# Optimization experiments

Measured on AMD Instinct MI355X. Metric: run time of the kernel, lower is better.

## Reference

```python
import jax, jax.numpy as jnp
import numpy as np

D_MODEL = 1024
N_HEADS = 16
D_HEAD = D_MODEL // N_HEADS
B, T = 4, 2048


def setup_inputs() -> dict:
    key = jax.random.key(0)
    k1, k2, k3 = jax.random.split(key, 3)
    x = jax.random.normal(k1, (B, T, D_MODEL), dtype=jnp.float32)
    # match nn.Linear init scale roughly (uniform ~ 1/sqrt(fan_in)); scale normal for stability
    w_qkv = jax.random.normal(k2, (D_MODEL, 3 * D_MODEL), dtype=jnp.float32) / np.sqrt(D_MODEL)
    w_out = jax.random.normal(k3, (D_MODEL, D_MODEL), dtype=jnp.float32) / np.sqrt(D_MODEL)
    return {"x": x, "w_qkv": w_qkv, "w_out": w_out}


def reference(x, w_qkv, w_out):
    Bx, Tx, D = x.shape
    H, Dh = N_HEADS, D_HEAD
    qkv = x @ w_qkv                                  # [B,T,3D]
    qkv = qkv.reshape(Bx, Tx, 3, H, Dh)
    q, k, v = qkv[:, :, 0], qkv[:, :, 1], qkv[:, :, 2]  # [B,T,H,Dh]
    scores = jnp.einsum('bqhd,bkhd->bhqk', q, k) / np.sqrt(Dh).astype(np.float32)
    mask = jnp.triu(jnp.ones((Tx, Tx), dtype=bool), k=1)  # causal: mask future
    scores = jnp.where(mask, -jnp.inf, scores)
    attn = jax.nn.softmax(scores, axis=-1)
    out = jnp.einsum('bhqk,bkhd->bqhd', attn, v).reshape(Bx, Tx, D)
    return out @ w_out
```

## Files before the change

### kernel.cpp

```cpp
#include <hip/hip_runtime.h>
#include <math.h>

#define T_SEQ 2048
#define NB 4
#define NH 16
#define DH 64
#define DM 1024

typedef __attribute__((ext_vector_type(8))) __bf16 bf16x8;
typedef __attribute__((ext_vector_type(4))) float f32x4;

typedef const __attribute__((address_space(1))) void* gas_t;
typedef __attribute__((address_space(3))) void* las_t;

#if __has_builtin(__builtin_amdgcn_exp2f)
#define EXP2(x) __builtin_amdgcn_exp2f(x)
#else
#define EXP2(x) __expf((x) * 0.69314718056f)
#endif

__device__ inline bool detect_f32(const unsigned short* probe, int lane) {
    unsigned short u = probe[lane];
    int e = (u >> 7) & 0xFF;
    bool outlier = (e >= 140) || (e <= 90 && (u & 0x7fff) != 0);
    unsigned long long m = __ballot(outlier);
    return __popcll(m) >= 4;
}

__device__ inline bf16x8 load8_flex(const void* base, long elem, bool f32) {
    if (!f32) {
        return *(const bf16x8*)((const __bf16*)base + elem);
    } else {
        const float* f = (const float*)base + elem;
        float4 a = *(const float4*)f;
        float4 b = *(const float4*)(f + 4);
        bf16x8 r;
        r[0] = (__bf16)a.x; r[1] = (__bf16)a.y; r[2] = (__bf16)a.z; r[3] = (__bf16)a.w;
        r[4] = (__bf16)b.x; r[5] = (__bf16)b.y; r[6] = (__bf16)b.z; r[7] = (__bf16)b.w;
        return r;
    }
}

__global__ __launch_bounds__(256)
void cvt_x(const float* __restrict__ in, __bf16* __restrict__ out, long n8) {
    long i = (long)blockIdx.x * blockDim.x + threadIdx.x;
    if (i >= n8) return;
    const float* f = in + i * 8;
    float4 a = *(const float4*)f;
    float4 b = *(const float4*)(f + 4);
    bf16x8 r;
    r[0] = (__bf16)a.x; r[1] = (__bf16)a.y; r[2] = (__bf16)a.z; r[3] = (__bf16)a.w;
    r[4] = (__bf16)b.x; r[5] = (__bf16)b.y; r[6] = (__bf16)b.z; r[7] = (__bf16)b.w;
    *(bf16x8*)(out + i * 8) = r;
}

__global__ __launch_bounds__(256)
void tpose_cvt(const float* __restrict__ in, __bf16* __restrict__ out, int R, int C) {
    __shared__ __bf16 tile[32][33];
    const int bx = blockIdx.x * 32;
    const int by = blockIdx.y * 32;
    const int tx = threadIdx.x & 31;
    const int ty = threadIdx.x >> 5;
#pragma unroll
    for (int it = 0; it < 4; ++it) {
        int r = ty + it * 8;
        tile[r][tx] = (__bf16)in[(long)(by + r) * C + bx + tx];
    }
    __syncthreads();
#pragma unroll
    for (int it = 0; it < 4; ++it) {
        int r = ty + it * 8;
        out[(long)(bx + r) * R + by + tx] = tile[tx][r];
    }
}

__global__ __launch_bounds__(256)
void gemm_bt(const __bf16* __restrict__ A, long lda,
             const __bf16* __restrict__ Bt, long ldb,
             void* __restrict__ C, long ldc, int c_f32, int K) {
    __shared__ __align__(16) __bf16 sA[128 * 32];
    __shared__ __align__(16) __bf16 sB[128 * 32];
    const int tid  = threadIdx.x;
    const int lane = tid & 63;
    const int wave = tid >> 6;
    const int l15  = lane & 15;
    const int quad = lane >> 4;

    const int wg   = blockIdx.x;
    const int xcd  = wg & 7;
    const int idx  = wg >> 3;
    const int bm = (xcd * 8 + (idx & 7)) * 128;
    const int bn = (idx >> 3) * 128;

    const int wm = (wave & 1) * 64;
    const int wn = (wave >> 1) * 64;

    f32x4 zero = {0.f, 0.f, 0.f, 0.f};
    f32x4 acc[4][4];
#pragma unroll
    for (int i = 0; i < 4; ++i)
#pragma unroll
        for (int j = 0; j < 4; ++j) acc[i][j] = zero;

    const int srow = tid >> 2;
    const int scol = (tid & 3) * 8;
    const __bf16* gA0 = A  + (long)(bm + srow) * lda + scol;
    const __bf16* gA1 = A  + (long)(bm + 64 + srow) * lda + scol;
    const __bf16* gB0 = Bt + (long)(bn + srow) * ldb + scol;
    const __bf16* gB1 = Bt + (long)(bn + 64 + srow) * ldb + scol;

    __bf16* lA0 = sA + wave * 512;
    __bf16* lA1 = sA + 2048 + wave * 512;
    __bf16* lB0 = sB + wave * 512;
    __bf16* lB1 = sB + 2048 + wave * 512;

    for (int k0 = 0; k0 < K; k0 += 32) {
        __syncthreads();
        __builtin_amdgcn_global_load_lds((gas_t)(gA0 + k0), (las_t)lA0, 16, 0, 0);
        __builtin_amdgcn_global_load_lds((gas_t)(gA1 + k0), (las_t)lA1, 16, 0, 0);
        __builtin_amdgcn_global_load_lds((gas_t)(gB0 + k0), (las_t)lB0, 16, 0, 0);
        __builtin_amdgcn_global_load_lds((gas_t)(gB1 + k0), (las_t)lB1, 16, 0, 0);
        __syncthreads();

        bf16x8 af[4], bfm[4];
#pragma unroll
        for (int i = 0; i < 4; ++i)
            af[i] = *(const bf16x8*)(sA + (wm + i * 16 + l15) * 32 + quad * 8);
#pragma unroll
        for (int j = 0; j < 4; ++j)
            bfm[j] = *(const bf16x8*)(sB + (wn + j * 16 + l15) * 32 + quad * 8);
#pragma unroll
        for (int i = 0; i < 4; ++i)
#pragma unroll
            for (int j = 0; j < 4; ++j)
                acc[i][j] = __builtin_amdgcn_mfma_f32_16x16x32_bf16(af[i], bfm[j], acc[i][j], 0, 0, 0);
    }

#pragma unroll
    for (int i = 0; i < 4; ++i)
#pragma unroll
        for (int j = 0; j < 4; ++j)
#pragma unroll
            for (int r = 0; r < 4; ++r) {
                int row = bm + wm + i * 16 + quad * 4 + r;
                int col = bn + wn + j * 16 + l15;
                if (c_f32)
                    ((float*)C)[(long)row * ldc + col] = acc[i][j][r];
                else
                    ((__bf16*)C)[(long)row * ldc + col] = (__bf16)acc[i][j][r];
            }
}

__global__ __launch_bounds__(256)
void gemm_bn(const void* __restrict__ A, long lda, long a0, int a_flex,
             const void* __restrict__ B, long ldb, int b_flex,
             void* __restrict__ C, long ldc, int c_flex, int K,
             const unsigned short* __restrict__ probe) {
    __shared__ __align__(16) __bf16 sA[128 * 32];
    __shared__ __align__(16) __bf16 sB[128 * 32];
    const int tid  = threadIdx.x;
    const int lane = tid & 63;
    const int wave = tid >> 6;
    const int l15  = lane & 15;
    const int quad = lane >> 4;
    const int bm = blockIdx.y * 128;
    const int bn = blockIdx.x * 128;
    const int wm = (wave & 1) * 64;
    const int wn = (wave >> 1) * 64;

    const bool is_f32 = detect_f32(probe, lane);
    const bool a_f32 = a_flex && is_f32;
    const bool b_f32 = b_flex && is_f32;
    const bool c_f32 = c_flex && is_f32;

    f32x4 zero = {0.f, 0.f, 0.f, 0.f};
    f32x4 acc[4][4];
#pragma unroll
    for (int i = 0; i < 4; ++i)
#pragma unroll
        for (int j = 0; j < 4; ++j) acc[i][j] = zero;

    const int srow = tid >> 2;
    const int scol = (tid & 3) * 8;

    for (int k0 = 0; k0 < K; k0 += 32) {
        __syncthreads();
        *(bf16x8*)(sA + tid * 8) =
            load8_flex(A, a0 + (long)(bm + srow) * lda + k0 + scol, a_f32);
        *(bf16x8*)(sA + 2048 + tid * 8) =
            load8_flex(A, a0 + (long)(bm + 64 + srow) * lda + k0 + scol, a_f32);
#pragma unroll
        for (int it = 0; it < 2; ++it) {
            int idx = tid + it * 256;
            int kk  = idx & 31;
            int n8  = (idx >> 5) * 8;
            bf16x8 bv = load8_flex(B, (long)(k0 + kk) * ldb + bn + n8, b_f32);
#pragma unroll
            for (int jj = 0; jj < 8; ++jj) sB[(n8 + jj) * 32 + kk] = bv[jj];
        }
        __syncthreads();

        bf16x8 af[4], bfm[4];
#pragma unroll
        for (int i = 0; i < 4; ++i)
            af[i] = *(const bf16x8*)(sA + (wm + i * 16 + l15) * 32 + quad * 8);
#pragma unroll
        for (int j = 0; j < 4; ++j)
            bfm[j] = *(const bf16x8*)(sB + (wn + j * 16 + l15) * 32 + quad * 8);
#pragma unroll
        for (int i = 0; i < 4; ++i)
#pragma unroll
            for (int j = 0; j < 4; ++j)
                acc[i][j] = __builtin_amdgcn_mfma_f32_16x16x32_bf16(af[i], bfm[j], acc[i][j], 0, 0, 0);
    }

#pragma unroll
    for (int i = 0; i < 4; ++i)
#pragma unroll
        for (int j = 0; j < 4; ++j)
#pragma unroll
            for (int r = 0; r < 4; ++r) {
                int row = bm + wm + i * 16 + quad * 4 + r;
                int col = bn + wn + j * 16 + l15;
                if (c_f32)
                    ((float*)C)[(long)row * ldc + col] = acc[i][j][r];
                else
                    ((__bf16*)C)[(long)row * ldc + col] = (__bf16)acc[i][j][r];
            }
}

__global__ __launch_bounds__(512, 4)
void attn_k(__bf16* __restrict__ qkvp, int bhbits) {
    const int bid  = blockIdx.x;
    const int p    = bid >> bhbits;
    const int bh   = bid & ((1 << bhbits) - 1);
    const int h    = bh & 15;
    const int b    = bh >> 4;
    const int tid  = threadIdx.x;
    const int lane = tid & 63;
    const int wave = tid >> 6;
    const int l15  = lane & 15;
    const int quad = lane >> 4;

    __shared__ __align__(16) __bf16 sK[64 * 72];
    __shared__ __align__(16) __bf16 sVT[64 * 64];
    __shared__ __align__(16) __bf16 sP[8][16 * 64];

    const long rs = 3 * DM;
    __bf16* base = qkvp + (long)b * T_SEQ * rs + h * DH;

    const int sr  = tid >> 3;
    const int sm  = tid & 7;
    const int sc8 = sm * 8;
    const int rot = 8 * ((5 * sm) & 7);
    const int vcol = (sr + rot) & 63;

    bf16x8 vone;
#pragma unroll
    for (int jj = 0; jj < 8; ++jj) vone[jj] = (__bf16)1.0f;

    f32x4 zero = {0.f, 0.f, 0.f, 0.f};

#pragma unroll 1
    for (int half = 0; half < 2; ++half) {
        const int qt  = half ? (15 - p) : p;
        const int q0  = qt * 128;
        const int wq0 = q0 + wave * 16;
        const int nk  = (q0 + 128) >> 6;

        const float qscale = 0.125f * 1.44269504089f;
        bf16x8 qa[2];
#pragma unroll
        for (int kk = 0; kk < 2; ++kk) {
            bf16x8 v = *(const bf16x8*)(base + (long)(wq0 + l15) * rs + kk * 32 + quad * 8);
#pragma unroll
            for (int jj = 0; jj < 8; ++jj) v[jj] = (__bf16)((float)v[jj] * qscale);
            qa[kk] = v;
        }

        f32x4 o[4], o4;
        o4 = zero;
#pragma unroll
        for (int j = 0; j < 4; ++j) o[j] = zero;

        bf16x8 kreg, vreg;
        {
            const __bf16* rp = base + (long)sr * rs;
            kreg = *(const bf16x8*)(rp + DM + sc8);
            vreg = *(const bf16x8*)(rp + 2 * DM + sc8);
        }

        for (int t = 0; t < nk; ++t) {
            const int k0 = t * 64;
            __syncthreads();
            *(bf16x8*)(sK + sr * 72 + sc8) = kreg;
#pragma unroll
            for (int jj = 0; jj < 8; ++jj)
                sVT[(sc8 + jj) * 64 + vcol] = vreg[jj];
            __syncthreads();

            if (t + 1 < nk) {
                const __bf16* rp = base + (long)(k0 + 64 + sr) * rs;
                kreg = *(const bf16x8*)(rp + DM + sc8);
                vreg = *(const bf16x8*)(rp + 2 * DM + sc8);
            }

            const bool active = (k0 <= wq0 + 15);
            if (active) {
                f32x4 s[4];
#pragma unroll
                for (int j = 0; j < 4; ++j) s[j] = zero;
#pragma unroll
                for (int kk = 0; kk < 2; ++kk) {
                    bf16x8 kb[4];
#pragma unroll
                    for (int j = 0; j < 4; ++j)
                        kb[j] = *(const bf16x8*)(sK + (j * 16 + l15) * 72 + kk * 32 + quad * 8);
#pragma unroll
                    for (int j = 0; j < 4; ++j)
                        s[j] = __builtin_amdgcn_mfma_f32_16x16x32_bf16(qa[kk], kb[j], s[j], 0, 0, 0);
                }

                const bool needmask = (k0 + 63 > wq0);
#pragma unroll
                for (int r = 0; r < 4; ++r) {
                    const int qg = wq0 + quad * 4 + r;
#pragma unroll
                    for (int j = 0; j < 4; ++j) {
                        const int kg = k0 + j * 16 + l15;
                        float pv = EXP2(fminf(s[j][r], 86.f));
                        if (needmask) pv = (kg > qg) ? 0.f : pv;
                        sP[wave][(quad * 4 + r) * 64 +
                                 ((j * 16 + l15 + 16 * quad) & 63)] = (__bf16)pv;
                    }
                }
            }

            __builtin_amdgcn_sched_barrier(0);
            __builtin_amdgcn_s_waitcnt(0xc07f);
            __builtin_amdgcn_sched_barrier(0);

            if (active) {
#pragma unroll
                for (int kk = 0; kk < 2; ++kk) {
                    bf16x8 pa, vb[4];
                    pa = *(const bf16x8*)(
                        &sP[wave][l15 * 64 +
                                  ((kk * 32 + quad * 8 + 16 * (l15 >> 2)) & 63)]);
#pragma unroll
                    for (int j = 0; j < 4; ++j) {
                        const int g = (2 * j + (l15 >> 3)) & 7;
                        vb[j] = *(const bf16x8*)(
                            sVT + (j * 16 + l15) * 64 +
                            ((kk * 32 + quad * 8 + 8 * ((5 * g) & 7)) & 63));
                    }
#pragma unroll
                    for (int j = 0; j < 4; ++j)
                        o[j] = __builtin_amdgcn_mfma_f32_16x16x32_bf16(pa, vb[j], o[j], 0, 0, 0);
                    o4 = __builtin_amdgcn_mfma_f32_16x16x32_bf16(pa, vone, o4, 0, 0, 0);
                }
            }
        }

#pragma unroll
        for (int r = 0; r < 4; ++r) {
            const int qg  = wq0 + quad * 4 + r;
            const float inv = 1.f / o4[r];
#pragma unroll
            for (int j = 0; j < 4; ++j)
                base[(long)qg * rs + j * 16 + l15] = (__bf16)(o[j][r] * inv);
        }
    }
}

__global__ __launch_bounds__(256)
void fallback_k(float* __restrict__ out, long n, float wsmb) {
    long i = (long)blockIdx.x * blockDim.x + threadIdx.x;
    for (; i < n; i += (long)gridDim.x * blockDim.x) out[i] = 0.f;
    if (blockIdx.x == 0 && threadIdx.x == 0) out[0] = wsmb;
}

extern "C" void kernel_launch(void* const* d_in, const int* in_sizes, int n_in,
                              void* d_out, int out_size, void* d_ws, size_t ws_size,
                              hipStream_t stream) {
    const void* x     = d_in[0];
    const void* w_qkv = d_in[1];
    const void* w_out = d_in[2];
    const unsigned short* probe = (const unsigned short*)d_in[0];

    __bf16* qkv = (__bf16*)d_ws;
    __bf16* xb  = qkv + (size_t)8192 * 3072;
    __bf16* wtq = xb  + (size_t)8192 * 1024;
    __bf16* wto = wtq + (size_t)3072 * 1024;

    const size_t NEED_T1   = (size_t)72 * 1024 * 1024;
    const size_t NEED_FULL = (size_t)8192 * 3072 * 2;
    const size_t NEED_B    = (size_t)2048 * 3072 * 2;

    if (ws_size >= NEED_T1) {
        cvt_x<<<dim3(4096), 256, 0, stream>>>((const float*)x, xb, (long)8192 * 1024 / 8);
        tpose_cvt<<<dim3(96, 32), 256, 0, stream>>>((const float*)w_qkv, wtq, 1024, 3072);
        tpose_cvt<<<dim3(32, 32), 256, 0, stream>>>((const float*)w_out, wto, 1024, 1024);
        gemm_bt<<<dim3(24 * 64), 256, 0, stream>>>(xb, 1024, wtq, 1024, qkv, 3072, 0, 1024);
        attn_k<<<dim3(8 * 64), 512, 0, stream>>>(qkv, 6);
        gemm_bt<<<dim3(8 * 64), 256, 0, stream>>>(qkv, 3072, wto, 1024, d_out, 1024, 1, 1024);
    } else if (ws_size >= NEED_FULL) {
        gemm_bn<<<dim3(24, 64), 256, 0, stream>>>(
            x, 1024, 0, 1, w_qkv, 3072, 1, qkv, 3072, 0, 1024, probe);
        attn_k<<<dim3(8 * 64), 512, 0, stream>>>(qkv, 6);
        gemm_bn<<<dim3(8, 64), 256, 0, stream>>>(
            qkv, 3072, 0, 0, w_out, 1024, 1, d_out, 1024, 1, 1024, probe);
    } else if (ws_size >= NEED_B) {
        for (int b = 0; b < NB; ++b) {
            long xoff = (long)b * T_SEQ * DM;
            gemm_bn<<<dim3(24, 16), 256, 0, stream>>>(
                x, 1024, xoff, 1, w_qkv, 3072, 1, qkv, 3072, 0, 1024, probe);
            attn_k<<<dim3(8 * 16), 512, 0, stream>>>(qkv, 4);
            gemm_bn<<<dim3(8, 16), 256, 0, stream>>>(
                qkv, 3072, 0, 0, w_out, 1024, 1,
                (void*)((char*)d_out + (size_t)b * T_SEQ * DM * 4),
                1024, 1, 1024, probe);
        }
    } else {
        fallback_k<<<dim3(512), 256, 0, stream>>>(
            (float*)d_out, (long)8192 * 1024, (float)(ws_size >> 20));
    }
}
```

Measured before the change: 273.8 us.

## Replace QKV GEMM with 256x256-tile, 4-stage pipelined 8-wave kernel

Adds gemm_8p, a 512-thread GEMM using 256x256 output tiles with a 4-deep LDS ring of global_load_lds stages, split half-step MFMA phases, explicit vmcnt/lgkmcnt waits, raw s_barrier and setprio, and uses it for the QKV projection. The goal is to overlap global loads with MFMA work and raise data reuse per tile compared with the single-buffered 128x128 gemm_bt, which syncs twice per k-step. It uses much more LDS and registers per block (8x4 accumulators per wave), which could limit occupancy, and the hand-tuned wait counts are fragile. The remaining edits are macro cleanups.

```diff
diff --git a/kernel.cpp b/kernel.cpp
--- a/kernel.cpp
+++ b/kernel.cpp
@@ -18,6 +18,12 @@
 #else
 #define EXP2(x) __expf((x) * 0.69314718056f)
 #endif
+
+#define SCHED0 __builtin_amdgcn_sched_barrier(0)
+#define GLD(src, dst) __builtin_amdgcn_global_load_lds((gas_t)(src), (las_t)(dst), 16, 0, 0)
+#define WAIT_VM(N) asm volatile("s_waitcnt vmcnt(" #N ")" ::: "memory")
+#define WAIT_LGKM0 asm volatile("s_waitcnt lgkmcnt(0)" ::: "memory")
+#define MEMFENCE   asm volatile("" ::: "memory")
 
 __device__ inline bool detect_f32(const unsigned short* probe, int lane) {
     unsigned short u = probe[lane];
@@ -74,6 +80,157 @@
     }
 }
 
+template<int NJ>
+__global__ __launch_bounds__(512, 2)
+void gemm_8p(const __bf16* __restrict__ A, long lda,
+             const __bf16* __restrict__ Bt, long ldb,
+             void* __restrict__ C, long ldc, int c_f32, int K, int nbn) {
+    constexpr int AUNIT = 256 * 32;
+    constexpr int BUNIT = NJ * 64 * 32;
+    constexpr int UNIT  = AUNIT + BUNIT;
+    __shared__ __align__(16) __bf16 lds[4 * UNIT];
+
+    const int tid  = threadIdx.x;
+    const int lane = tid & 63;
+    const int wave = tid >> 6;
+    const int l15  = lane & 15;
+    const int quad = lane >> 4;
+
+    const int wg  = blockIdx.x;
+    const int cpx = gridDim.x >> 3;
+    const int swz = (wg & 7) * cpx + (wg >> 3);
+    const int bm  = (swz / nbn) * 256;
+    const int bn  = (swz % nbn) * (NJ * 64);
+
+    const int wm = (wave & 1) * 128;
+    const int wn = (wave >> 1) * (NJ * 16);
+
+    f32x4 zero = {0.f, 0.f, 0.f, 0.f};
+    f32x4 acc[8][NJ];
+#pragma unroll
+    for (int i = 0; i < 8; ++i)
+#pragma unroll
+        for (int j = 0; j < NJ; ++j) acc[i][j] = zero;
+
+    const int srow = lane >> 2;
+    const int scol = (lane & 3) * 8;
+    const __bf16* aS = A  + (long)(bm + wave * 32 + srow) * lda + scol;
+    const __bf16* bS = Bt + (long)(bn + wave * (NJ == 4 ? 32 : 16) + srow) * ldb + scol;
+
+    const int NHALF = K >> 5;
+
+#pragma unroll
+    for (int u = 0; u < 3; ++u) {
+        __bf16* LA = lds + u * UNIT;
+        __bf16* LB = LA + AUNIT;
+        const __bf16* sa = aS + u * 32;
+        GLD(sa,            LA + (wave * 2 + 0) * 512);
+        GLD(sa + 16 * lda, LA + (wave * 2 + 1) * 512);
+        const __bf16* sb = bS + u * 32;
+        if constexpr (NJ == 4) {
+            GLD(sb,            LB + (wave * 2 + 0) * 512);
+            GLD(sb + 16 * ldb, LB + (wave * 2 + 1) * 512);
+        } else {
+            GLD(sb, LB + wave * 512);
+        }
+    }
+    SCHED0;
+    if constexpr (NJ == 4) WAIT_VM(8); else WAIT_VM(6);
+    SCHED0;
+    __builtin_amdgcn_s_barrier();
+    SCHED0;
+
+    for (int h = 0; h < NHALF; ++h) {
+        const __bf16* uA = lds + (h & 3) * UNIT;
+        const __bf16* uB = uA + AUNIT;
+        __bf16* wA = lds + ((h + 3) & 3) * UNIT;
+        __bf16* wB = wA + AUNIT;
+        const bool st = (h + 3) < NHALF;
+        const long kc = (long)(h + 3) * 32;
+
+        bf16x8 af[4], bf[NJ];
+
+#pragma unroll
+        for (int i = 0; i < 4; ++i)
+            af[i] = *(const bf16x8*)(uA + (wm + i * 16 + l15) * 32 + quad * 8);
+#pragma unroll
+        for (int j = 0; j < NJ; ++j)
+            bf[j] = *(const bf16x8*)(uB + (wn + j * 16 + l15) * 32 + quad * 8);
+        if (st) {
+            const __bf16* sa = aS + kc;
+            GLD(sa,            wA + (wave * 2 + 0) * 512);
+            GLD(sa + 16 * lda, wA + (wave * 2 + 1) * 512);
+        }
+        MEMFENCE;
+        __builtin_amdgcn_s_barrier();
+        SCHED0;
+        WAIT_LGKM0;
+        SCHED0;
+        __builtin_amdgcn_s_setprio(1);
+#pragma unroll
+        for (int i = 0; i < 4; ++i)
+#pragma unroll
+            for (int j = 0; j < NJ; ++j)
+                acc[i][j] = __builtin_amdgcn_mfma_f32_16x16x32_bf16(af[i], bf[j], acc[i][j], 0, 0, 0);
+        __builtin_amdgcn_s_setprio(0);
+        MEMFENCE;
+        __builtin_amdgcn_s_barrier();
+        SCHED0;
+
+#pragma unroll
+        for (int i = 0; i < 4; ++i)
+            af[i] = *(const bf16x8*)(uA + (wm + (i + 4) * 16 + l15) * 32 + quad * 8);
+        if (st) {
+            const __bf16* sb = bS + kc;
+            if constexpr (NJ == 4) {
+                GLD(sb,            wB + (wave * 2 + 0) * 512);
+                GLD(sb + 16 * ldb, wB + (wave * 2 + 1) * 512);
+            } else {
+                GLD(sb, wB + wave * 512);
+            }
+        }
+        SCHED0;
+        if constexpr (NJ == 4) {
+            if (h <= NHALF - 4)      WAIT_VM(8);
+            else if (h == NHALF - 3) WAIT_VM(4);
+            else                     WAIT_VM(0);
+        } else {
+            if (h <= NHALF - 4)      WAIT_VM(6);
+            else if (h == NHALF - 3) WAIT_VM(3);
+            else                     WAIT_VM(0);
+        }
+        SCHED0;
+        __builtin_amdgcn_s_barrier();
+        SCHED0;
+        WAIT_LGKM0;
+        SCHED0;
+        __builtin_amdgcn_s_setprio(1);
+#pragma unroll
+        for (int i = 0; i < 4; ++i)
+#pragma unroll
+            for (int j = 0; j < NJ; ++j)
+                acc[i + 4][j] = __builtin_amdgcn_mfma_f32_16x16x32_bf16(af[i], bf[j], acc[i + 4][j], 0, 0, 0);
+        __builtin_amdgcn_s_setprio(0);
+        MEMFENCE;
+        __builtin_amdgcn_s_barrier();
+        SCHED0;
+    }
+
+#pragma unroll
+    for (int i = 0; i < 8; ++i)
+#pragma unroll
+        for (int j = 0; j < NJ; ++j)
+#pragma unroll
+            for (int r = 0; r < 4; ++r) {
+                int row = bm + wm + i * 16 + quad * 4 + r;
+                int col = bn + wn + j * 16 + l15;
+                if (c_f32)
+                    ((float*)C)[(long)row * ldc + col] = acc[i][j][r];
+                else
+                    ((__bf16*)C)[(long)row * ldc + col] = (__bf16)acc[i][j][r];
+            }
+}
+
 __global__ __launch_bounds__(256)
 void gemm_bt(const __bf16* __restrict__ A, long lda,
              const __bf16* __restrict__ Bt, long ldb,
@@ -116,10 +273,10 @@
 
     for (int k0 = 0; k0 < K; k0 += 32) {
         __syncthreads();
-        __builtin_amdgcn_global_load_lds((gas_t)(gA0 + k0), (las_t)lA0, 16, 0, 0);
-        __builtin_amdgcn_global_load_lds((gas_t)(gA1 + k0), (las_t)lA1, 16, 0, 0);
-        __builtin_amdgcn_global_load_lds((gas_t)(gB0 + k0), (las_t)lB0, 16, 0, 0);
-        __builtin_amdgcn_global_load_lds((gas_t)(gB1 + k0), (las_t)lB1, 16, 0, 0);
+        GLD(gA0 + k0, lA0);
+        GLD(gA1 + k0, lA1);
+        GLD(gB0 + k0, lB0);
+        GLD(gB1 + k0, lB1);
         __syncthreads();
 
         bf16x8 af[4], bfm[4];
@@ -336,9 +493,9 @@
                 }
             }
 
-            __builtin_amdgcn_sched_barrier(0);
-            __builtin_amdgcn_s_waitcnt(0xc07f);
-            __builtin_amdgcn_sched_barrier(0);
+            SCHED0;
+            WAIT_LGKM0;
+            SCHED0;
 
             if (active) {
 #pragma unroll
@@ -401,7 +558,7 @@
         cvt_x<<<dim3(4096), 256, 0, stream>>>((const float*)x, xb, (long)8192 * 1024 / 8);
         tpose_cvt<<<dim3(96, 32), 256, 0, stream>>>((const float*)w_qkv, wtq, 1024, 3072);
         tpose_cvt<<<dim3(32, 32), 256, 0, stream>>>((const float*)w_out, wto, 1024, 1024);
-        gemm_bt<<<dim3(24 * 64), 256, 0, stream>>>(xb, 1024, wtq, 1024, qkv, 3072, 0, 1024);
+        gemm_8p<4><<<dim3(384), 512, 0, stream>>>(xb, 1024, wtq, 1024, qkv, 3072, 0, 1024, 12);
         attn_k<<<dim3(8 * 64), 512, 0, stream>>>(qkv, 6);
         gemm_bt<<<dim3(8 * 64), 256, 0, stream>>>(qkv, 3072, wto, 1024, d_out, 1024, 1, 1024);
     } else if (ws_size >= NEED_FULL) {
```

Measured after the change: 270.2 us. Within noise of the previous version (-1.3%).

## Rewrite projection GEMM with 4-stage LDS ring, 128x256 tiles and swizzled loads

Applied to the files above, without the earlier changes.

The GEMM kernel now uses 8 waves per block on a 128x256 output tile. A four-slot LDS ring buffer prefetches three K-chunks ahead with direct global-to-LDS loads, and a single barrier per iteration replaces the old two-syncthreads pattern. LDS columns are XOR-swizzled to reduce bank conflicts, and MFMA sections run at raised wave priority. The goal is to hide global memory latency and raise reuse per tile, at the cost of more LDS per block, which may lower occupancy. The attention wait is also rewritten as an lgkmcnt(0) wait.

```diff
diff --git a/kernel.cpp b/kernel.cpp
--- a/kernel.cpp
+++ b/kernel.cpp
@@ -18,6 +18,12 @@
 #else
 #define EXP2(x) __expf((x) * 0.69314718056f)
 #endif
+
+#define SCHED0 __builtin_amdgcn_sched_barrier(0)
+#define GLD(src, dst) __builtin_amdgcn_global_load_lds((gas_t)(src), (las_t)(dst), 16, 0, 0)
+#define WAIT_VM(N) asm volatile("s_waitcnt vmcnt(" #N ")" ::: "memory")
+#define WAIT_LGKM0 asm volatile("s_waitcnt lgkmcnt(0)" ::: "memory")
+#define MEMFENCE   asm volatile("" ::: "memory")
 
 __device__ inline bool detect_f32(const unsigned short* probe, int lane) {
     unsigned short u = probe[lane];
@@ -74,12 +80,15 @@
     }
 }
 
-__global__ __launch_bounds__(256)
-void gemm_bt(const __bf16* __restrict__ A, long lda,
+__global__ __launch_bounds__(512, 2)
+void gemm_8p(const __bf16* __restrict__ A, long lda,
              const __bf16* __restrict__ Bt, long ldb,
              void* __restrict__ C, long ldc, int c_f32, int K) {
-    __shared__ __align__(16) __bf16 sA[128 * 32];
-    __shared__ __align__(16) __bf16 sB[128 * 32];
+    constexpr int AUNIT = 128 * 32;
+    constexpr int BUNIT = 256 * 32;
+    constexpr int UNIT  = AUNIT + BUNIT;
+    __shared__ __align__(16) __bf16 lds[4 * UNIT];
+
     const int tid  = threadIdx.x;
     const int lane = tid & 63;
     const int wave = tid >> 6;
@@ -89,8 +98,8 @@
     const int wg   = blockIdx.x;
     const int xcd  = wg & 7;
     const int idx  = wg >> 3;
-    const int bm = (xcd * 8 + (idx & 7)) * 128;
-    const int bn = (idx >> 3) * 128;
+    const int bm   = (xcd * 8 + (idx & 7)) * 128;
+    const int bn   = (idx >> 3) * 256;
 
     const int wm = (wave & 1) * 64;
     const int wn = (wave >> 1) * 64;
@@ -102,38 +111,67 @@
 #pragma unroll
         for (int j = 0; j < 4; ++j) acc[i][j] = zero;
 
-    const int srow = tid >> 2;
-    const int scol = (tid & 3) * 8;
-    const __bf16* gA0 = A  + (long)(bm + srow) * lda + scol;
-    const __bf16* gA1 = A  + (long)(bm + 64 + srow) * lda + scol;
-    const __bf16* gB0 = Bt + (long)(bn + srow) * ldb + scol;
-    const __bf16* gB1 = Bt + (long)(bn + 64 + srow) * ldb + scol;
-
-    __bf16* lA0 = sA + wave * 512;
-    __bf16* lA1 = sA + 2048 + wave * 512;
-    __bf16* lB0 = sB + wave * 512;
-    __bf16* lB1 = sB + 2048 + wave * 512;
-
-    for (int k0 = 0; k0 < K; k0 += 32) {
-        __syncthreads();
-        __builtin_amdgcn_global_load_lds((gas_t)(gA0 + k0), (las_t)lA0, 16, 0, 0);
-        __builtin_amdgcn_global_load_lds((gas_t)(gA1 + k0), (las_t)lA1, 16, 0, 0);
-        __builtin_amdgcn_global_load_lds((gas_t)(gB0 + k0), (las_t)lB0, 16, 0, 0);
-        __builtin_amdgcn_global_load_lds((gas_t)(gB1 + k0), (las_t)lB1, 16, 0, 0);
-        __syncthreads();
-
-        bf16x8 af[4], bfm[4];
+    const int srow  = lane >> 2;
+    const int swcol = ((lane & 3) ^ ((lane >> 3) & 3)) * 8;
+    const __bf16* aS = A  + (long)(bm + wave * 16 + srow) * lda + swcol;
+    const __bf16* bS = Bt + (long)(bn + wave * 32 + srow) * ldb + swcol;
+
+    const int rsel = ((l15 >> 1) & 3);
+    const int rcol = ((quad ^ rsel) * 8);
+
+    const int NHALF = K >> 5;
+
+#pragma unroll
+    for (int u = 0; u < 3; ++u) {
+        __bf16* wU = lds + u * UNIT;
+        const long kc = (long)u * 32;
+        GLD(aS + kc,            wU + wave * 512);
+        GLD(bS + kc,            wU + AUNIT + (wave * 2 + 0) * 512);
+        GLD(bS + 16 * ldb + kc, wU + AUNIT + (wave * 2 + 1) * 512);
+    }
+    SCHED0;
+    WAIT_VM(6);
+    SCHED0;
+    __builtin_amdgcn_s_barrier();
+    SCHED0;
+
+    for (int h = 0; h < NHALF; ++h) {
+        const __bf16* uA = lds + (h & 3) * UNIT;
+        const __bf16* uB = uA + AUNIT;
+        __bf16* wU = lds + ((h + 3) & 3) * UNIT;
+
+        bf16x8 af[4], bf[4];
 #pragma unroll
         for (int i = 0; i < 4; ++i)
-            af[i] = *(const bf16x8*)(sA + (wm + i * 16 + l15) * 32 + quad * 8);
+            af[i] = *(const bf16x8*)(uA + (wm + i * 16 + l15) * 32 + rcol);
 #pragma unroll
         for (int j = 0; j < 4; ++j)
-            bfm[j] = *(const bf16x8*)(sB + (wn + j * 16 + l15) * 32 + quad * 8);
+            bf[j] = *(const bf16x8*)(uB + (wn + j * 16 + l15) * 32 + rcol);
+
+        if (h + 3 < NHALF) {
+            const long kc = (long)(h + 3) * 32;
+            GLD(aS + kc,            wU + wave * 512);
+            GLD(bS + kc,            wU + AUNIT + (wave * 2 + 0) * 512);
+            GLD(bS + 16 * ldb + kc, wU + AUNIT + (wave * 2 + 1) * 512);
+        }
+        SCHED0;
+        WAIT_LGKM0;
+        SCHED0;
+        __builtin_amdgcn_s_setprio(1);
 #pragma unroll
         for (int i = 0; i < 4; ++i)
 #pragma unroll
             for (int j = 0; j < 4; ++j)
-                acc[i][j] = __builtin_amdgcn_mfma_f32_16x16x32_bf16(af[i], bfm[j], acc[i][j], 0, 0, 0);
+                acc[i][j] = __builtin_amdgcn_mfma_f32_16x16x32_bf16(af[i], bf[j], acc[i][j], 0, 0, 0);
+        __builtin_amdgcn_s_setprio(0);
+        SCHED0;
+        if (h < NHALF - 3)       WAIT_VM(6);
+        else if (h == NHALF - 3) WAIT_VM(3);
+        else                     WAIT_VM(0);
+        SCHED0;
+        MEMFENCE;
+        __builtin_amdgcn_s_barrier();
+        SCHED0;
     }
 
 #pragma unroll
@@ -336,9 +374,9 @@
                 }
             }
 
-            __builtin_amdgcn_sched_barrier(0);
-            __builtin_amdgcn_s_waitcnt(0xc07f);
-            __builtin_amdgcn_sched_barrier(0);
+            SCHED0;
+            WAIT_LGKM0;
+            SCHED0;
 
             if (active) {
 #pragma unroll
@@ -401,9 +439,9 @@
         cvt_x<<<dim3(4096), 256, 0, stream>>>((const float*)x, xb, (long)8192 * 1024 / 8);
         tpose_cvt<<<dim3(96, 32), 256, 0, stream>>>((const float*)w_qkv, wtq, 1024, 3072);
         tpose_cvt<<<dim3(32, 32), 256, 0, stream>>>((const float*)w_out, wto, 1024, 1024);
-        gemm_bt<<<dim3(24 * 64), 256, 0, stream>>>(xb, 1024, wtq, 1024, qkv, 3072, 0, 1024);
+        gemm_8p<<<dim3(768), 512, 0, stream>>>(xb, 1024, wtq, 1024, qkv, 3072, 0, 1024);
         attn_k<<<dim3(8 * 64), 512, 0, stream>>>(qkv, 6);
-        gemm_bt<<<dim3(8 * 64), 256, 0, stream>>>(qkv, 3072, wto, 1024, d_out, 1024, 1, 1024);
+        gemm_8p<<<dim3(256), 512, 0, stream>>>(qkv, 3072, wto, 1024, d_out, 1024, 1, 1024);
     } else if (ws_size >= NEED_FULL) {
         gemm_bn<<<dim3(24, 64), 256, 0, stream>>>(
             x, 1024, 0, 1, w_qkv, 3072, 1, qkv, 3072, 0, 1024, probe);
```

Measured after the change: 259.7 us. 1.05x faster.
